# Performance work log

Measured on AMD Instinct MI355X. Metric: run time of the kernel, lower is better.

The kernel has to match this reference:

```python
import jax, jax.numpy as jnp
import numpy as np

NEG_SLOPE = 0.01  # nn.LeakyReLU default


def _quantize_weight(w, bits):
    """Brevitas-style per-tensor symmetric narrow-range weight quantization.
    scale = max|w| / (2^(bits-1)-1); w_q = clip(round(w/scale)) * scale."""
    n = float(2 ** (bits - 1) - 1)
    scale = jnp.max(jnp.abs(w)) / n
    q = jnp.clip(jnp.round(w / scale), -n, n)
    return q * scale


def setup_inputs() -> dict:
    key = jax.random.key(0)
    ks = jax.random.split(key, 7)
    N, D_in, D_out = 32768, 1024, 2048
    x = jax.random.normal(ks[0], (N, D_in), dtype=jnp.float32)
    # He-ish init scaling for stability
    W0 = jax.random.normal(ks[1], (D_out, D_in), dtype=jnp.float32) * (1.0 / np.sqrt(D_in))
    b0 = jax.random.normal(ks[2], (D_out,), dtype=jnp.float32) * 0.01
    W1 = jax.random.normal(ks[3], (D_out, D_out), dtype=jnp.float32) * (1.0 / np.sqrt(D_out))
    b1 = jax.random.normal(ks[4], (D_out,), dtype=jnp.float32) * 0.01
    W2 = jax.random.normal(ks[5], (D_out, D_out), dtype=jnp.float32) * (1.0 / np.sqrt(D_out))
    b2 = jax.random.normal(ks[6], (D_out,), dtype=jnp.float32) * 0.01
    return {"x": x, "W0": W0, "b0": b0, "W1": W1, "b1": b1, "W2": W2, "b2": b2}


def reference(x, W0, b0, W1, b1, W2, b2):
    # Layer 0: QuantLinear with default 8-bit weights, then LeakyReLU, dropout(p=0)=id
    h = jnp.dot(x, _quantize_weight(W0, 8).T) + b0
    h = jnp.where(h >= 0, h, NEG_SLOPE * h)
    # Layers 1..2: 4-bit quantized weights
    for W, b in ((W1, b1), (W2, b2)):
        h = jnp.dot(h, _quantize_weight(W, 4).T) + b
        h = jnp.where(h >= 0, h, NEG_SLOPE * h)
    return h
```

## Files before the change

### kernel.cpp

```cpp
#include <hip/hip_runtime.h>
#include <hip/hip_bf16.h>
#include <stdint.h>

typedef __bf16 bf16x8 __attribute__((ext_vector_type(8)));
typedef float  f32x4  __attribute__((ext_vector_type(4)));
typedef unsigned short u16;

__device__ __forceinline__ u16 f2bf(float f) {
    return __builtin_bit_cast(u16, __float2bfloat16(f));
}

__device__ __forceinline__ void gload16(const void* g, void* l) {
    __builtin_amdgcn_global_load_lds(
        (const __attribute__((address_space(1))) void*)g,
        (__attribute__((address_space(3))) void*)l,
        16, 0, 0);
}


__global__ void zero3_k(unsigned int* p) {
    if (threadIdx.x < 3) p[threadIdx.x] = 0u;
}

__global__ void maxabs_k(const float* __restrict__ w, int n, unsigned int* __restrict__ out) {
    const int tid = threadIdx.x;
    float m = 0.f;
    for (int i = blockIdx.x * blockDim.x + tid; i < n; i += gridDim.x * blockDim.x)
        m = fmaxf(m, fabsf(w[i]));
    #pragma unroll
    for (int off = 32; off > 0; off >>= 1)
        m = fmaxf(m, __shfl_down(m, off));
    __shared__ float red[4];
    if ((tid & 63) == 0) red[tid >> 6] = m;
    __syncthreads();
    if (tid == 0) {
        m = fmaxf(fmaxf(red[0], red[1]), fmaxf(red[2], red[3]));
        atomicMax(out, __float_as_uint(m));
    }
}

__global__ void quant_k(const float* __restrict__ w, int n,
                        const unsigned int* __restrict__ maxbits, float qn,
                        u16* __restrict__ out) {
    const float scale = __uint_as_float(*maxbits) / qn;
    for (int i = blockIdx.x * blockDim.x + threadIdx.x; i < n; i += gridDim.x * blockDim.x) {
        float q = rintf(w[i] / scale);
        q = fminf(qn, fmaxf(-qn, q));
        out[i] = f2bf(q * scale);
    }
}

__global__ void cvt_k(const float* __restrict__ x, u16* __restrict__ o, long n) {
    const long stride = (long)gridDim.x * blockDim.x * 4;
    for (long i = ((long)blockIdx.x * blockDim.x + threadIdx.x) * 4; i < n; i += stride) {
        float4 v = *(const float4*)(x + i);
        unsigned int lo = (unsigned int)f2bf(v.x) | ((unsigned int)f2bf(v.y) << 16);
        unsigned int hi = (unsigned int)f2bf(v.z) | ((unsigned int)f2bf(v.w) << 16);
        *(uint2*)(o + i) = make_uint2(lo, hi);
    }
}


#define BARR  __builtin_amdgcn_s_barrier()
#define LGKM0 do { asm volatile("s_waitcnt lgkmcnt(0)" ::: "memory");          \
                   __builtin_amdgcn_sched_barrier(0); } while (0)
#define FENCE asm volatile("" ::: "memory")

#define STG(kt, ISA, h)                                                        \
  do {                                                                         \
    const u16* _s = (ISA) ? gA : gB;                                           \
    u16* _d = smem + ((ISA) ? 0 : 32768) + (((kt) & 1) << 14) + ((h) << 13)    \
              + wave * 512;                                                    \
    const size_t _go = (size_t)((h) * 128) * K + (size_t)(kt) * 64;            \
    gload16(_s + _go,                 _d);                                     \
    gload16(_s + _go + (size_t)64 * K, _d + 4096);                             \
  } while (0)

#define RD_A(kt, mh)                                                           \
  do {                                                                         \
    const u16* _p = smem + (((kt) & 1) << 14) + ((mh) << 13) + rowA;           \
    _Pragma("unroll") for (int m2 = 0; m2 < 4; ++m2) {                         \
        afr[m2 * 2]     = *(const bf16x8*)(_p + m2 * 2048 + g0);               \
        afr[m2 * 2 + 1] = *(const bf16x8*)(_p + m2 * 2048 + g1);               \
    }                                                                          \
  } while (0)

#define RD_B(kt, nh, DST)                                                      \
  do {                                                                         \
    const u16* _p = smem + 32768 + (((kt) & 1) << 14) + ((nh) << 13) + rowB;   \
    _Pragma("unroll") for (int n2 = 0; n2 < 2; ++n2) {                         \
        DST[n2 * 2]     = *(const bf16x8*)(_p + n2 * 4096 + g0);               \
        DST[n2 * 2 + 1] = *(const bf16x8*)(_p + n2 * 4096 + g1);               \
    }                                                                          \
  } while (0)

#define MM(mh, nh, BS)                                                         \
  do {                                                                         \
    __builtin_amdgcn_s_setprio(1);                                             \
    _Pragma("unroll") for (int m2 = 0; m2 < 4; ++m2)                           \
      _Pragma("unroll") for (int n2 = 0; n2 < 2; ++n2) {                       \
        acc[(mh)*4+m2][(nh)*2+n2] = __builtin_amdgcn_mfma_f32_16x16x32_bf16(   \
            afr[m2*2],     BS[n2*2],   acc[(mh)*4+m2][(nh)*2+n2], 0, 0, 0);    \
        acc[(mh)*4+m2][(nh)*2+n2] = __builtin_amdgcn_mfma_f32_16x16x32_bf16(   \
            afr[m2*2+1],   BS[n2*2+1], acc[(mh)*4+m2][(nh)*2+n2], 0, 0, 0);    \
      }                                                                        \
    __builtin_amdgcn_s_setprio(0);                                             \
  } while (0)

#define KTILE(kt, VMSTR, DO_STAGE)                                             \
  do {                                                                         \
    FENCE; BARR; FENCE;          \
    if (DO_STAGE) { STG((kt)+1, 1, 0); STG((kt)+1, 0, 0);                      \
                    STG((kt)+1, 0, 1); STG((kt)+1, 1, 1); }                    \
    asm volatile("s_waitcnt vmcnt(" VMSTR ")" ::: "memory");                   \
    FENCE; BARR; FENCE;          \
    RD_A(kt, 0); RD_B(kt, 0, b0f);                                             \
    LGKM0;                                                                     \
    MM(0, 0, b0f);                                                             \
    RD_B(kt, 1, b1f);                                                          \
    LGKM0;                                                                     \
    MM(0, 1, b1f);                                                             \
    RD_A(kt, 1);                                                               \
    LGKM0;                                                                     \
    MM(1, 0, b0f);                                                             \
    __builtin_amdgcn_sched_barrier(0);                                         \
    MM(1, 1, b1f);                                                             \
  } while (0)

template<int BF16OUT>
__global__ __launch_bounds__(512, 2)
void gemm8x(const u16* __restrict__ A, const u16* __restrict__ B,
            const float* __restrict__ bias, void* __restrict__ Cv,
            int M, int Nn, int K)
{
    __shared__ __align__(128) u16 smem[65536];

    const int tid  = threadIdx.x;
    const int lane = tid & 63;
    const int wave = tid >> 6;
    const int wm = wave >> 2;
    const int wn = wave & 3;

    const int nbx = Nn >> 8;
    const int cpx = gridDim.x >> 3;
    const int swz = (blockIdx.x & 7) * cpx + (blockIdx.x >> 3);
    const int bn = (swz % nbx) << 8;
    const int bm = (swz / nbx) << 8;

    const int scol = (((tid & 7) ^ ((tid >> 4) & 7)) << 3);
    const u16* gA = A + (size_t)(bm + (tid >> 3)) * K + scol;
    const u16* gB = B + (size_t)(bn + (tid >> 3)) * K + scol;

    const int fr = lane & 15;
    const int g0 = (((lane >> 4)    ) ^ (fr >> 1)) << 3;
    const int g1 = (((lane >> 4) + 4) ^ (fr >> 1)) << 3;
    const int rowA = (wm * 16 + fr) << 6;
    const int rowB = (wn * 16 + fr) << 6;

    f32x4 acc[8][4] = {};
    bf16x8 afr[8], b0f[4], b1f[4];

    const int NT = K >> 6;

    STG(0, 1, 0); STG(0, 0, 0); STG(0, 0, 1); STG(0, 1, 1);

    for (int kt = 0; kt < NT - 1; ++kt)
        KTILE(kt, "8", true);
    KTILE(NT - 1, "0", false);

    const int crow = (lane >> 4) << 2;
    const int ccol = lane & 15;
    #pragma unroll
    for (int n = 0; n < 4; ++n) {
        const int col = bn + n * 64 + wn * 16 + ccol;
        const float bv = bias[col];
        #pragma unroll
        for (int m = 0; m < 8; ++m) {
            const int row0 = bm + (m >> 2) * 128 + (m & 3) * 32 + wm * 16 + crow;
            #pragma unroll
            for (int j = 0; j < 4; ++j) {
                float v = acc[m][n][j] + bv;
                v = (v >= 0.f) ? v : 0.01f * v;
                if (BF16OUT) {
                    ((u16*)Cv)[(size_t)(row0 + j) * Nn + col] = f2bf(v);
                } else {
                    ((float*)Cv)[(size_t)(row0 + j) * Nn + col] = v;
                }
            }
        }
    }
}


extern "C" void kernel_launch(void* const* d_in, const int* in_sizes, int n_in,
                              void* d_out, int out_size, void* d_ws, size_t ws_size,
                              hipStream_t stream) {
    const float* x  = (const float*)d_in[0];
    const float* W0 = (const float*)d_in[1];
    const float* b0 = (const float*)d_in[2];
    const float* W1 = (const float*)d_in[3];
    const float* b1 = (const float*)d_in[4];
    const float* W2 = (const float*)d_in[5];
    const float* b2 = (const float*)d_in[6];

    const int N = 32768, D0 = 1024, D1 = 2048;

    char* ws = (char*)d_ws;
    u16* xbf = (u16*)ws;  ws += (size_t)N * D0 * 2;
    u16* h0  = (u16*)ws;  ws += (size_t)N * D1 * 2;
    u16* h1  = (u16*)ws;  ws += (size_t)N * D1 * 2;
    u16* w0q = (u16*)ws;  ws += (size_t)D1 * D0 * 2;
    u16* w1q = (u16*)ws;  ws += (size_t)D1 * D1 * 2;
    u16* w2q = (u16*)ws;  ws += (size_t)D1 * D1 * 2;
    unsigned int* scales = (unsigned int*)ws;

    zero3_k<<<1, 64, 0, stream>>>(scales);
    maxabs_k<<<256, 256, 0, stream>>>(W0, D1 * D0, scales + 0);
    maxabs_k<<<256, 256, 0, stream>>>(W1, D1 * D1, scales + 1);
    maxabs_k<<<256, 256, 0, stream>>>(W2, D1 * D1, scales + 2);
    quant_k<<<2048, 256, 0, stream>>>(W0, D1 * D0, scales + 0, 127.f, w0q);
    quant_k<<<2048, 256, 0, stream>>>(W1, D1 * D1, scales + 1, 7.f, w1q);
    quant_k<<<2048, 256, 0, stream>>>(W2, D1 * D1, scales + 2, 7.f, w2q);
    cvt_k<<<4096, 256, 0, stream>>>(x, xbf, (long)N * D0);

    const int blocks = (D1 / 256) * (N / 256);
    gemm8x<1><<<blocks, 512, 0, stream>>>(xbf, w0q, b0, h0, N, D1, D0);
    gemm8x<1><<<blocks, 512, 0, stream>>>(h0, w1q, b1, h1, N, D1, D1);
    gemm8x<0><<<blocks, 512, 0, stream>>>(h1, w2q, b2, d_out, N, D1, D1);
}
```

Measured before the change: 810.0 us.

## Prepack quantized weights into MFMA fragment layout and load B directly to registers

The weight quantization kernel now writes bf16 weights in a fragment-packed layout, so each wave can load its B operand straight from global memory into registers with coalesced 16-byte loads. B staging through LDS is removed, which halves shared memory use and drops the B LDS reads and waits. B loads are double-buffered in registers across k-tiles to overlap with the MFMAs. The costs are higher register pressure and direct global-load latency on B, with reuse now coming from L2 instead of LDS.

```diff
diff --git a/kernel.cpp b/kernel.cpp
--- a/kernel.cpp
+++ b/kernel.cpp
@@ -39,14 +39,27 @@
     }
 }
 
-__global__ void quant_k(const float* __restrict__ w, int n,
-                        const unsigned int* __restrict__ maxbits, float qn,
-                        u16* __restrict__ out) {
+__global__ void quant_pack_k(const float* __restrict__ w, int rows, int K, int l2k8,
+                             const unsigned int* __restrict__ maxbits, float qn,
+                             u16* __restrict__ out) {
     const float scale = __uint_as_float(*maxbits) / qn;
-    for (int i = blockIdx.x * blockDim.x + threadIdx.x; i < n; i += gridDim.x * blockDim.x) {
-        float q = rintf(w[i] / scale);
-        q = fminf(qn, fmaxf(-qn, q));
-        out[i] = f2bf(q * scale);
+    const int nchunk = rows * (K >> 3);
+    const int NB16 = rows >> 4;
+    for (int i = blockIdx.x * blockDim.x + threadIdx.x; i < nchunk;
+         i += gridDim.x * blockDim.x) {
+        const int r  = i >> l2k8;
+        const int k8 = i & ((1 << l2k8) - 1);
+        const float* src = w + (size_t)r * K + (k8 << 3);
+        u16 tmp[8];
+        #pragma unroll
+        for (int j = 0; j < 8; ++j) {
+            float q = rintf(src[j] / scale);
+            q = fminf(qn, fmaxf(-qn, q));
+            tmp[j] = f2bf(q * scale);
+        }
+        const size_t chunk = ((size_t)(k8 >> 2) * NB16 + (r >> 4)) * 64
+                             + (r & 15) + ((k8 & 3) << 4);
+        *(uint4*)(out + chunk * 8) = *(const uint4*)tmp;
     }
 }
 
@@ -66,14 +79,22 @@
                    __builtin_amdgcn_sched_barrier(0); } while (0)
 #define FENCE asm volatile("" ::: "memory")
 
-#define STG(kt, ISA, h)                                                        \
-  do {                                                                         \
-    const u16* _s = (ISA) ? gA : gB;                                           \
-    u16* _d = smem + ((ISA) ? 0 : 32768) + (((kt) & 1) << 14) + ((h) << 13)    \
-              + wave * 512;                                                    \
+#define STG(kt, h)                                                             \
+  do {                                                                         \
+    u16* _d = smem + (((kt) & 1) << 14) + ((h) << 13) + wave * 512;            \
     const size_t _go = (size_t)((h) * 128) * K + (size_t)(kt) * 64;            \
-    gload16(_s + _go,                 _d);                                     \
-    gload16(_s + _go + (size_t)64 * K, _d + 4096);                             \
+    gload16(gA + _go,                  _d);                                    \
+    gload16(gA + _go + (size_t)64 * K, _d + 4096);                             \
+  } while (0)
+
+#define LOAD_B(kt, D0, D1)                                                     \
+  do {                                                                         \
+    const u16* _p = pBb + (size_t)(2 * (kt)) * kStrideB;                       \
+    _Pragma("unroll") for (int ks = 0; ks < 2; ++ks)                           \
+      _Pragma("unroll") for (int n2 = 0; n2 < 2; ++n2) {                       \
+        D0[n2 * 2 + ks] = *(const bf16x8*)(_p + ks * kStrideB + n2 * 2048);    \
+        D1[n2 * 2 + ks] = *(const bf16x8*)(_p + ks * kStrideB + 4096 + n2 * 2048);\
+      }                                                                        \
   } while (0)
 
 #define RD_A(kt, mh)                                                           \
@@ -82,15 +103,6 @@
     _Pragma("unroll") for (int m2 = 0; m2 < 4; ++m2) {                         \
         afr[m2 * 2]     = *(const bf16x8*)(_p + m2 * 2048 + g0);               \
         afr[m2 * 2 + 1] = *(const bf16x8*)(_p + m2 * 2048 + g1);               \
-    }                                                                          \
-  } while (0)
-
-#define RD_B(kt, nh, DST)                                                      \
-  do {                                                                         \
-    const u16* _p = smem + 32768 + (((kt) & 1) << 14) + ((nh) << 13) + rowB;   \
-    _Pragma("unroll") for (int n2 = 0; n2 < 2; ++n2) {                         \
-        DST[n2 * 2]     = *(const bf16x8*)(_p + n2 * 4096 + g0);               \
-        DST[n2 * 2 + 1] = *(const bf16x8*)(_p + n2 * 4096 + g1);               \
     }                                                                          \
   } while (0)
 
@@ -107,33 +119,31 @@
     __builtin_amdgcn_s_setprio(0);                                             \
   } while (0)
 
-#define KTILE(kt, VMSTR, DO_STAGE)                                             \
-  do {                                                                         \
-    FENCE; BARR; FENCE;          \
-    if (DO_STAGE) { STG((kt)+1, 1, 0); STG((kt)+1, 0, 0);                      \
-                    STG((kt)+1, 0, 1); STG((kt)+1, 1, 1); }                    \
+#define KTILE(kt, VMSTR, DO_STAGE, CUR0, CUR1, NXT0, NXT1)                     \
+  do {                                                                         \
+    FENCE; BARR; FENCE;               \
+    if (DO_STAGE) { STG((kt)+1, 0); STG((kt)+1, 1);                            \
+                    LOAD_B((kt)+1, NXT0, NXT1); }                              \
     asm volatile("s_waitcnt vmcnt(" VMSTR ")" ::: "memory");                   \
-    FENCE; BARR; FENCE;          \
-    RD_A(kt, 0); RD_B(kt, 0, b0f);                                             \
+    FENCE; BARR; FENCE;                        \
+    RD_A(kt, 0);                                                               \
     LGKM0;                                                                     \
-    MM(0, 0, b0f);                                                             \
-    RD_B(kt, 1, b1f);                                                          \
-    LGKM0;                                                                     \
-    MM(0, 1, b1f);                                                             \
+    MM(0, 0, CUR0);                                                            \
+    MM(0, 1, CUR1);                                                            \
     RD_A(kt, 1);                                                               \
     LGKM0;                                                                     \
-    MM(1, 0, b0f);                                                             \
+    MM(1, 0, CUR0);                                                            \
     __builtin_amdgcn_sched_barrier(0);                                         \
-    MM(1, 1, b1f);                                                             \
+    MM(1, 1, CUR1);                                                            \
   } while (0)
 
 template<int BF16OUT>
 __global__ __launch_bounds__(512, 2)
-void gemm8x(const u16* __restrict__ A, const u16* __restrict__ B,
+void gemmbr(const u16* __restrict__ A, const u16* __restrict__ pB,
             const float* __restrict__ bias, void* __restrict__ Cv,
             int M, int Nn, int K)
 {
-    __shared__ __align__(128) u16 smem[65536];
+    __shared__ __align__(128) u16 smem[32768];
 
     const int tid  = threadIdx.x;
     const int lane = tid & 63;
@@ -149,24 +159,32 @@
 
     const int scol = (((tid & 7) ^ ((tid >> 4) & 7)) << 3);
     const u16* gA = A + (size_t)(bm + (tid >> 3)) * K + scol;
-    const u16* gB = B + (size_t)(bn + (tid >> 3)) * K + scol;
+
+    const int NB16 = Nn >> 4;
+    const size_t kStrideB = (size_t)NB16 * 512;
+    const u16* pBb = pB + ((size_t)((bn >> 4) + wn)) * 512 + (lane << 3);
 
     const int fr = lane & 15;
     const int g0 = (((lane >> 4)    ) ^ (fr >> 1)) << 3;
     const int g1 = (((lane >> 4) + 4) ^ (fr >> 1)) << 3;
     const int rowA = (wm * 16 + fr) << 6;
-    const int rowB = (wn * 16 + fr) << 6;
 
     f32x4 acc[8][4] = {};
-    bf16x8 afr[8], b0f[4], b1f[4];
+    bf16x8 afr[8], cB0[4], cB1[4], nB0[4], nB1[4];
 
     const int NT = K >> 6;
 
-    STG(0, 1, 0); STG(0, 0, 0); STG(0, 0, 1); STG(0, 1, 1);
-
-    for (int kt = 0; kt < NT - 1; ++kt)
-        KTILE(kt, "8", true);
-    KTILE(NT - 1, "0", false);
+    STG(0, 0); STG(0, 1);
+    LOAD_B(0, cB0, cB1);
+    asm volatile("s_waitcnt vmcnt(8)" ::: "memory");
+    BARR;
+
+    for (int kt = 0; kt < NT - 2; kt += 2) {
+        KTILE(kt,     "12", true, cB0, cB1, nB0, nB1);
+        KTILE(kt + 1, "12", true, nB0, nB1, cB0, cB1);
+    }
+    KTILE(NT - 2, "12", true, cB0, cB1, nB0, nB1);
+    KTILE(NT - 1, "0",  false, nB0, nB1, cB0, cB1);
 
     const int crow = (lane >> 4) << 2;
     const int ccol = lane & 15;
@@ -218,13 +236,13 @@
     maxabs_k<<<256, 256, 0, stream>>>(W0, D1 * D0, scales + 0);
     maxabs_k<<<256, 256, 0, stream>>>(W1, D1 * D1, scales + 1);
     maxabs_k<<<256, 256, 0, stream>>>(W2, D1 * D1, scales + 2);
-    quant_k<<<2048, 256, 0, stream>>>(W0, D1 * D0, scales + 0, 127.f, w0q);
-    quant_k<<<2048, 256, 0, stream>>>(W1, D1 * D1, scales + 1, 7.f, w1q);
-    quant_k<<<2048, 256, 0, stream>>>(W2, D1 * D1, scales + 2, 7.f, w2q);
+    quant_pack_k<<<2048, 256, 0, stream>>>(W0, D1, D0, 7, scales + 0, 127.f, w0q);
+    quant_pack_k<<<2048, 256, 0, stream>>>(W1, D1, D1, 8, scales + 1, 7.f, w1q);
+    quant_pack_k<<<2048, 256, 0, stream>>>(W2, D1, D1, 8, scales + 2, 7.f, w2q);
     cvt_k<<<4096, 256, 0, stream>>>(x, xbf, (long)N * D0);
 
     const int blocks = (D1 / 256) * (N / 256);
-    gemm8x<1><<<blocks, 512, 0, stream>>>(xbf, w0q, b0, h0, N, D1, D0);
-    gemm8x<1><<<blocks, 512, 0, stream>>>(h0, w1q, b1, h1, N, D1, D1);
-    gemm8x<0><<<blocks, 512, 0, stream>>>(h1, w2q, b2, d_out, N, D1, D1);
-}
+    gemmbr<1><<<blocks, 512, 0, stream>>>(xbf, w0q, b0, h0, N, D1, D0);
+    gemmbr<1><<<blocks, 512, 0, stream>>>(h0, w1q, b1, h1, N, D1, D1);
+    gemmbr<0><<<blocks, 512, 0, stream>>>(h1, w2q, b2, d_out, N, D1, D1);
+}
```

New measurement: 945.7 us. 1.17x slower.
